# Performance work log

Measured on AMD Instinct MI355X. Metric: run time of the kernel, lower is better.

Reference implementation:

```python
import jax, jax.numpy as jnp
import numpy as np
from jax import lax

BN_INV = float(1.0 / np.sqrt(1.0 + 1e-5))  # BatchNorm eval: running_mean=0, running_var=1


def _block(x, w, b, g, beta, stride):
    # Conv3x3(stride, pad=1) -> BN(eval) -> ReLU -> MaxPool2
    x = lax.conv_general_dilated(x, w, (stride, stride), [(1, 1), (1, 1)],
                                 dimension_numbers=('NCHW', 'OIHW', 'NCHW'))
    x = x + b[None, :, None, None]
    x = x * (g * BN_INV)[None, :, None, None] + beta[None, :, None, None]
    x = jax.nn.relu(x)
    return lax.reduce_window(x, -jnp.inf, lax.max, (1, 1, 2, 2), (1, 1, 2, 2), 'VALID')


def _gru(x, wi, wh, bi, bh):
    # torch-style GRU, batch_first. x: (B, T, D)
    B = x.shape[0]
    H = wh.shape[1]

    def step(h, xt):
        gi = xt @ wi.T + bi
        gh = h @ wh.T + bh
        ir, iz, inn = jnp.split(gi, 3, axis=1)
        hr, hz, hn = jnp.split(gh, 3, axis=1)
        r = jax.nn.sigmoid(ir + hr)
        z = jax.nn.sigmoid(iz + hz)
        nn_ = jnp.tanh(inn + r * hn)
        h2 = (1.0 - z) * nn_ + z * h
        return h2, h2

    h0 = jnp.zeros((B, H), x.dtype)
    _, ys = lax.scan(step, h0, jnp.swapaxes(x, 0, 1))
    return jnp.swapaxes(ys, 0, 1)  # (B, T, H)


def setup_inputs() -> dict:
    key = jax.random.key(0)
    ks = jax.random.split(key, 32)
    rn = lambda i, shape, s: jax.random.normal(ks[i], shape, jnp.float32) * s
    inp = {
        'support': rn(0, (5, 5, 1, 224, 224), 1.0),
        'query': rn(1, (15, 1, 224, 224), 1.0),
        'conv_w1': rn(2, (32, 1, 3, 3), 0.3), 'conv_b1': rn(3, (32,), 0.1),
        'conv_w2': rn(4, (64, 32, 3, 3), 0.06), 'conv_b2': rn(5, (64,), 0.1),
        'conv_w3': rn(6, (128, 64, 3, 3), 0.04), 'conv_b3': rn(7, (128,), 0.1),
        'conv_w4': rn(8, (256, 128, 3, 3), 0.03), 'conv_b4': rn(9, (256,), 0.1),
        'bn_g1': 1.0 + rn(10, (32,), 0.05), 'bn_be1': rn(11, (32,), 0.05),
        'bn_g2': 1.0 + rn(12, (64,), 0.05), 'bn_be2': rn(13, (64,), 0.05),
        'bn_g3': 1.0 + rn(14, (128,), 0.05), 'bn_be3': rn(15, (128,), 0.05),
        'bn_g4': 1.0 + rn(16, (256,), 0.05), 'bn_be4': rn(17, (256,), 0.05),
        'att_w': rn(18, (64, 256), 0.06), 'att_b': rn(19, (64,), 0.05),
        'gru_wi0': rn(20, (384, 512), 0.04), 'gru_wh0': rn(21, (384, 128), 0.08),
        'gru_bi0': rn(22, (384,), 0.05), 'gru_bh0': rn(23, (384,), 0.05),
        'gru_wi1': rn(24, (384, 128), 0.08), 'gru_wh1': rn(25, (384, 128), 0.08),
        'gru_bi1': rn(26, (384,), 0.05), 'gru_bh1': rn(27, (384,), 0.05),
        'trans_w': rn(28, (1, 128), 0.08), 'trans_b': rn(29, (1,), 0.05),
    }
    return inp


def reference(support, query, conv_w1, conv_b1, conv_w2, conv_b2, conv_w3, conv_b3,
              conv_w4, conv_b4, bn_g1, bn_be1, bn_g2, bn_be2, bn_g3, bn_be3,
              bn_g4, bn_be4, att_w, att_b, gru_wi0, gru_wh0, gru_bi0, gru_bh0,
              gru_wi1, gru_wh1, gru_bi1, gru_bh1, trans_w, trans_b):
    n, k, c, w = support.shape[0], support.shape[1], support.shape[2], support.shape[3]
    qk = query.shape[0]

    def enc(x):
        x = _block(x, conv_w1, conv_b1, bn_g1, bn_be1, 2)
        x = _block(x, conv_w2, conv_b2, bn_g2, bn_be2, 1)
        x = _block(x, conv_w3, conv_b3, bn_g3, bn_be3, 1)
        x = _block(x, conv_w4, conv_b4, bn_g4, bn_be4, 1)
        B, F_, H_, W_ = x.shape
        return x.reshape(B, F_, H_ * W_).transpose(0, 2, 1)  # (B, seq, feat)

    hf = enc(support.reshape(n * k, c, w, w))  # (nk, S, f)
    qf = enc(query)                            # (qk, T, f)

    # ItemQueryAttention: score[q,s,t,u] = sum_h tanh(W(q_t) * W(h_u))
    Wq = qf @ att_w.T + att_b  # (qk, T, h)
    Wh = hf @ att_w.T + att_b  # (nk, S, h)
    scores = jnp.tanh(Wq[:, None, :, None, :] * Wh[None, :, None, :, :]).sum(-1)  # (qk,nk,T,S)
    att = jax.nn.softmax(scores, axis=3)
    attended = jnp.einsum('qsTS,sSf->qsTf', att, hf)  # (qk, nk, T, f)

    T_, f = qf.shape[1], qf.shape[2]
    qrep = jnp.broadcast_to(qf[:, None], (qk, n * k, T_, f))
    x = jnp.concatenate([attended, qrep], axis=-1).reshape(qk * n * k, T_, 2 * f)

    h = _gru(x, gru_wi0, gru_wh0, gru_bi0, gru_bh0)
    h = _gru(h, gru_wi1, gru_wh1, gru_bi1, gru_bh1)

    logits = (h[:, -1, :] @ trans_w.T + trans_b).reshape(qk, n, k).sum(axis=2)  # (qk, n)
    return jax.nn.log_softmax(logits, axis=1)
```

## Files before the change

kernel.cpp:

```cpp
#include <hip/hip_runtime.h>
#include <hip/hip_bf16.h>
#include <math.h>

typedef unsigned short u16;
typedef unsigned int u32;
typedef __attribute__((ext_vector_type(8))) short bf16x8v;
typedef __attribute__((ext_vector_type(4))) float f32x4;

constexpr int NS = 25, NQ = 15, NB = 40;
constexpr int B3 = 375;
constexpr int T49 = 49;
constexpr float BN_INV = 0.9999950000374997f;

constexpr size_t A1_OFF    = 0;
constexpr size_t X2_OFF    = 16056320;
constexpr size_t P2_OFF    = 48168960;
constexpr size_t X3_OFF    = 0;
constexpr size_t P3_OFF    = 56197120;
constexpr size_t X4_OFF    = 16056320;
constexpr size_t FEATT_OFF = 60211200;
constexpr size_t PROJ_OFF  = 24084480;
constexpr size_t ATT_OFF   = 24586240;
constexpr size_t GI_OFF    = 62218240;
constexpr size_t Y0_OFF    = 0;
constexpr size_t HFIN_OFF  = 90442240;
constexpr size_t WBH_OFF   = 91027456;
constexpr size_t WBL_OFF   = 92325888;
constexpr size_t W2_E = 0;
constexpr size_t W3_E = 18432;
constexpr size_t W4_E = 92160;
constexpr size_t AW_E = 387072;
constexpr size_t WI0_E = 403456;
constexpr size_t WI1_E = 600064;

static __device__ __forceinline__ u16 f2b(float f) {
  __hip_bfloat16 h = __float2bfloat16(f);
  return *reinterpret_cast<u16*>(&h);
}
static __device__ __forceinline__ float b2f(u16 u) {
  return __uint_as_float((u32)u << 16);
}
static __device__ __forceinline__ void split8(const float* v, u32* hp, u32* lp) {
  u16 h[8], l[8];
#pragma unroll
  for (int j = 0; j < 8; ++j) {
    const u16 hb = f2b(v[j]);
    h[j] = hb;
    l[j] = f2b(v[j] - b2f(hb));
  }
#pragma unroll
  for (int j = 0; j < 4; ++j) {
    hp[j] = (u32)h[2 * j] | ((u32)h[2 * j + 1] << 16);
    lp[j] = (u32)l[2 * j] | ((u32)l[2 * j + 1] << 16);
  }
}
constexpr float LOG2E = 1.4426950408889634f;
static __device__ __forceinline__ float fsigmoid(float x) {
  return __builtin_amdgcn_rcpf(1.f + __builtin_amdgcn_exp2f(-x * LOG2E));
}
static __device__ __forceinline__ float ftanh(float x) {
  return 1.f - 2.f * __builtin_amdgcn_rcpf(__builtin_amdgcn_exp2f(x * (2.f * LOG2E)) + 1.f);
}

__global__ void cvt_split(const float* __restrict__ x, u16* __restrict__ oh,
                          u16* __restrict__ ol, int n) {
  int i = blockIdx.x * 256 + threadIdx.x;
  if (i >= n) return;
  const float v = x[i];
  const u16 h = f2b(v);
  oh[i] = h;
  ol[i] = f2b(v - b2f(h));
}
__global__ void cvt_conv_w_split(const float* __restrict__ w, u16* __restrict__ oh,
                                 u16* __restrict__ ol, int OC, int IC) {
  const int n = OC * IC * 9;
  int i = blockIdx.x * 256 + threadIdx.x;
  if (i >= n) return;
  const int oc = i / (IC * 9), rem = i % (IC * 9);
  const int e = rem / IC, ic = rem % IC;
  const int ky = e / 3, kx = e % 3;
  const float v = w[((size_t)(oc * IC + ic) * 3 + ky) * 3 + kx];
  const u16 h = f2b(v);
  oh[i] = h;
  ol[i] = f2b(v - b2f(h));
}

__global__ __launch_bounds__(256) void conv1_pool(
    const float* __restrict__ support, const float* __restrict__ query,
    const float* __restrict__ w1, const float* __restrict__ cb1,
    const float* __restrict__ g1, const float* __restrict__ be1,
    float* __restrict__ out) {
  __shared__ float wl[288], scl[32], shl[32], cbl[32];
  const int tid = threadIdx.x;
  for (int l = tid; l < 288; l += 256) wl[l] = w1[l];
  if (tid < 32) { scl[tid] = g1[tid] * BN_INV; shl[tid] = be1[tid]; cbl[tid] = cb1[tid]; }
  __syncthreads();
  const int oc = tid & 31;
  const int p = blockIdx.x * 8 + (tid >> 5);
  const int ox = p % 56, oy = (p / 56) % 56, b = p / 3136;
  const float* in_b = (b < NS) ? (support + (size_t)b * 50176)
                               : (query + (size_t)(b - NS) * 50176);
  const int iy0 = 4 * oy - 1, ix0 = 4 * ox - 1;
  float pat[5][5];
#pragma unroll
  for (int dy = 0; dy < 5; ++dy) {
    const int iy = iy0 + dy;
#pragma unroll
    for (int dx = 0; dx < 5; ++dx) {
      const int ix = ix0 + dx;
      pat[dy][dx] = (iy >= 0 && iy < 224 && ix >= 0 && ix < 224)
                        ? in_b[(size_t)iy * 224 + ix] : 0.f;
    }
  }
  const float* wp = &wl[oc * 9];
  float mx = 0.f;
#pragma unroll
  for (int py = 0; py < 2; ++py)
#pragma unroll
    for (int px = 0; px < 2; ++px) {
      float acc = 0.f;
#pragma unroll
      for (int ky = 0; ky < 3; ++ky)
#pragma unroll
        for (int kx = 0; kx < 3; ++kx)
          acc += pat[2 * py + ky][2 * px + kx] * wp[ky * 3 + kx];
      float v = (acc + cbl[oc]) * scl[oc] + shl[oc];
      mx = fmaxf(mx, v);
    }
  out[(size_t)p * 32 + oc] = mx;
}

__global__ void maxpool2_f32(const float* __restrict__ X, float* __restrict__ Y,
                             int Bn, int H, int W, int C) {
  const int OH = H >> 1, OW = W >> 1;
  const int cpr = C >> 2;
  const int chunks = Bn * OH * OW * cpr;
  for (int i = blockIdx.x * blockDim.x + threadIdx.x; i < chunks;
       i += gridDim.x * blockDim.x) {
    const int c4 = i % cpr, m = i / cpr;
    const int ox = m % OW, oy = (m / OW) % OH, b = m / (OW * OH);
    const size_t base = (((size_t)b * H + 2 * oy) * W + 2 * ox) * C + (c4 << 2);
    const float4 r0 = *(const float4*)&X[base];
    const float4 r1 = *(const float4*)&X[base + C];
    const float4 r2 = *(const float4*)&X[base + (size_t)W * C];
    const float4 r3 = *(const float4*)&X[base + (size_t)W * C + C];
    float4 o;
    o.x = fmaxf(fmaxf(r0.x, r1.x), fmaxf(r2.x, r3.x));
    o.y = fmaxf(fmaxf(r0.y, r1.y), fmaxf(r2.y, r3.y));
    o.z = fmaxf(fmaxf(r0.z, r1.z), fmaxf(r2.z, r3.z));
    o.w = fmaxf(fmaxf(r0.w, r1.w), fmaxf(r2.w, r3.w));
    *(float4*)&Y[(size_t)m * C + (c4 << 2)] = o;
  }
}

template <int AMODE, int EPI>
__global__ __launch_bounds__(256) void sgemm(
    const float* __restrict__ A, const float* __restrict__ A2, int M, int K,
    const u16* __restrict__ Bh, const u16* __restrict__ Bl,
    const float* __restrict__ p0, const float* __restrict__ p1,
    const float* __restrict__ p2, float* __restrict__ Cout, int ldc,
    int H, int W, int IC, int icb) {
  __shared__ u16 Ash[64][72], Asl[64][72];
  __shared__ u16 Bsh[64][72], Bsl[64][72];
  const int tid = threadIdx.x;
  const int lane = tid & 63, wv = tid >> 6;
  const int wy = wv >> 1, wx = wv & 1;
  const int n0 = blockIdx.x * 64, m0 = blockIdx.y * 64;
  f32x4 acc[2][2] = {{{0, 0, 0, 0}, {0, 0, 0, 0}}, {{0, 0, 0, 0}, {0, 0, 0, 0}}};
  for (int k0 = 0; k0 < K; k0 += 64) {
#pragma unroll
    for (int s = 0; s < 2; ++s) {
      const int c = s * 256 + tid;
      const int row = c >> 3, kc = (c & 7) << 3;
      const int gm = m0 + row, gk = k0 + kc;
      float4 x0 = {0, 0, 0, 0}, x1 = {0, 0, 0, 0};
      if (AMODE == 0) {
        if (gm < M && gk < K) {
          const float* p = A + (size_t)gm * K + gk;
          x0 = *(const float4*)p; x1 = *(const float4*)(p + 4);
        }
      } else if (AMODE == 1) {
        if (gm < M) {
          const float* p;
          if (gk < 256) {
            p = A + (size_t)gm * 256 + gk;
          } else {
            const int b = gm / T49, t = gm % T49, q = b / NS;
            p = A2 + (((size_t)(NS + q) * T49 + t) << 8) + (gk - 256);
          }
          x0 = *(const float4*)p; x1 = *(const float4*)(p + 4);
        }
      } else {
        if (gm < M && gk < K) {
          const int ox = gm % W, t_ = gm / W;
          const int oy = t_ % H, b = t_ / H;
          const int e = gk >> icb, ic = gk & (IC - 1);
          const int ky = e / 3, kx = e - 3 * (e / 3);
          const int iy = oy + ky - 1, ix = ox + kx - 1;
          if (iy >= 0 && iy < H && ix >= 0 && ix < W) {
            const float* p = A + (((size_t)b * H + iy) * W + ix) * IC + ic;
            x0 = *(const float4*)p; x1 = *(const float4*)(p + 4);
          }
        }
      }
      float v[8] = {x0.x, x0.y, x0.z, x0.w, x1.x, x1.y, x1.z, x1.w};
      u32 hp[4], lp[4];
      split8(v, hp, lp);
      *(uint4*)&Ash[row][kc] = *(uint4*)hp;
      *(uint4*)&Asl[row][kc] = *(uint4*)lp;
    }
#pragma unroll
    for (int s = 0; s < 2; ++s) {
      const int c = s * 256 + tid;
      const int row = c >> 3, kc = (c & 7) << 3;
      const int gk = k0 + kc;
      uint4 vh = {0u, 0u, 0u, 0u}, vl = {0u, 0u, 0u, 0u};
      if (gk < K) {
        vh = *(const uint4*)&Bh[(size_t)(n0 + row) * K + gk];
        vl = *(const uint4*)&Bl[(size_t)(n0 + row) * K + gk];
      }
      *(uint4*)&Bsh[row][kc] = vh;
      *(uint4*)&Bsl[row][kc] = vl;
    }
    __syncthreads();
#pragma unroll
    for (int kk = 0; kk < 64; kk += 32) {
      const int ko = kk + ((lane >> 4) << 3);
      const int ra0 = wy * 32 + (lane & 15), ra1 = ra0 + 16;
      const int rb0 = wx * 32 + (lane & 15), rb1 = rb0 + 16;
      bf16x8v a0h = *(const bf16x8v*)&Ash[ra0][ko];
      bf16x8v a1h = *(const bf16x8v*)&Ash[ra1][ko];
      bf16x8v b0h = *(const bf16x8v*)&Bsh[rb0][ko];
      bf16x8v b1h = *(const bf16x8v*)&Bsh[rb1][ko];
      bf16x8v a0l = *(const bf16x8v*)&Asl[ra0][ko];
      bf16x8v a1l = *(const bf16x8v*)&Asl[ra1][ko];
      bf16x8v b0l = *(const bf16x8v*)&Bsl[rb0][ko];
      bf16x8v b1l = *(const bf16x8v*)&Bsl[rb1][ko];
      acc[0][0] = __builtin_amdgcn_mfma_f32_16x16x32_bf16(a0h, b0h, acc[0][0], 0, 0, 0);
      acc[0][1] = __builtin_amdgcn_mfma_f32_16x16x32_bf16(a0h, b1h, acc[0][1], 0, 0, 0);
      acc[1][0] = __builtin_amdgcn_mfma_f32_16x16x32_bf16(a1h, b0h, acc[1][0], 0, 0, 0);
      acc[1][1] = __builtin_amdgcn_mfma_f32_16x16x32_bf16(a1h, b1h, acc[1][1], 0, 0, 0);
      acc[0][0] = __builtin_amdgcn_mfma_f32_16x16x32_bf16(a0h, b0l, acc[0][0], 0, 0, 0);
      acc[0][1] = __builtin_amdgcn_mfma_f32_16x16x32_bf16(a0h, b1l, acc[0][1], 0, 0, 0);
      acc[1][0] = __builtin_amdgcn_mfma_f32_16x16x32_bf16(a1h, b0l, acc[1][0], 0, 0, 0);
      acc[1][1] = __builtin_amdgcn_mfma_f32_16x16x32_bf16(a1h, b1l, acc[1][1], 0, 0, 0);
      acc[0][0] = __builtin_amdgcn_mfma_f32_16x16x32_bf16(a0l, b0h, acc[0][0], 0, 0, 0);
      acc[0][1] = __builtin_amdgcn_mfma_f32_16x16x32_bf16(a0l, b1h, acc[0][1], 0, 0, 0);
      acc[1][0] = __builtin_amdgcn_mfma_f32_16x16x32_bf16(a1l, b0h, acc[1][0], 0, 0, 0);
      acc[1][1] = __builtin_amdgcn_mfma_f32_16x16x32_bf16(a1l, b1h, acc[1][1], 0, 0, 0);
    }
    __syncthreads();
  }
#pragma unroll
  for (int r = 0; r < 2; ++r) {
#pragma unroll
    for (int c = 0; c < 2; ++c) {
      const int gn = n0 + wx * 32 + c * 16 + (lane & 15);
      float sc0 = 0.f, sh0 = 0.f;
      if (EPI == 0) { sc0 = p1[gn] * BN_INV; sh0 = p2[gn]; }
#pragma unroll
      for (int i = 0; i < 4; ++i) {
        const int gm = m0 + wy * 32 + r * 16 + ((lane >> 4) << 2) + i;
        if (gm >= M) continue;
        const float a = acc[r][c][i];
        if (EPI == 0) {
          Cout[(size_t)gm * ldc + gn] = fmaxf((a + p0[gn]) * sc0 + sh0, 0.f);
        } else {
          Cout[(size_t)gm * ldc + gn] = a + p0[gn];
        }
      }
    }
  }
}

__global__ __launch_bounds__(256) void attention_f32(
    const float* __restrict__ proj, const float* __restrict__ featT,
    float* __restrict__ attended) {
  __shared__ float WqT[64][9];
  __shared__ float WhT[64][51];
  __shared__ float sc[7][64];
  const int bid = blockIdx.x;
  const int qs = bid / 7, tg = bid - 7 * qs;
  const int q = qs / NS, s = qs - NS * q;
  const int tid = threadIdx.x;
  const float* pq = proj + ((size_t)(NS + q) * T49 + tg * 7) * 64;
  const float* ph = proj + (size_t)s * T49 * 64;
  for (int l = tid; l < 7 * 64; l += 256) WqT[l & 63][l >> 6] = pq[l];
  for (int l = tid; l < T49 * 64; l += 256) WhT[l & 63][l >> 6] = ph[l];
  __syncthreads();
  constexpr float C2LOG2E = 2.8853900817779268f;
  for (int e = tid; e < 343; e += 256) {
    const int tl = e / 49, u = e - 49 * tl;
    float a0 = 0.f, a1 = 0.f, a2 = 0.f, a3 = 0.f;
#pragma unroll
    for (int h = 0; h < 64; h += 4) {
      const float p0 = WqT[h + 0][tl] * WhT[h + 0][u];
      const float p1 = WqT[h + 1][tl] * WhT[h + 1][u];
      const float p2 = WqT[h + 2][tl] * WhT[h + 2][u];
      const float p3 = WqT[h + 3][tl] * WhT[h + 3][u];
      a0 += 1.f - 2.f * __builtin_amdgcn_rcpf(__builtin_amdgcn_exp2f(p0 * C2LOG2E) + 1.f);
      a1 += 1.f - 2.f * __builtin_amdgcn_rcpf(__builtin_amdgcn_exp2f(p1 * C2LOG2E) + 1.f);
      a2 += 1.f - 2.f * __builtin_amdgcn_rcpf(__builtin_amdgcn_exp2f(p2 * C2LOG2E) + 1.f);
      a3 += 1.f - 2.f * __builtin_amdgcn_rcpf(__builtin_amdgcn_exp2f(p3 * C2LOG2E) + 1.f);
    }
    sc[tl][u] = (a0 + a1) + (a2 + a3);
  }
  __syncthreads();
  if (tid < 56) {
    const int t = tid >> 3, g = tid & 7;
    float m = -3.4e38f;
    for (int u = g; u < T49; u += 8) m = fmaxf(m, sc[t][u]);
    m = fmaxf(m, __shfl_xor(m, 4));
    m = fmaxf(m, __shfl_xor(m, 2));
    m = fmaxf(m, __shfl_xor(m, 1));
    float ssum = 0.f;
    for (int u = g; u < T49; u += 8) {
      const float e = __builtin_amdgcn_exp2f((sc[t][u] - m) * LOG2E);
      sc[t][u] = e; ssum += e;
    }
    ssum += __shfl_xor(ssum, 4);
    ssum += __shfl_xor(ssum, 2);
    ssum += __shfl_xor(ssum, 1);
    const float inv = 1.f / ssum;
    for (int u = g; u < T49; u += 8) sc[t][u] *= inv;
  }
  __syncthreads();
  const float* fs = featT + (size_t)s * T49 * 256;
  float* outp = attended + ((size_t)qs * T49 + tg * 7) * 256;
  float acc[7] = {0.f, 0.f, 0.f, 0.f, 0.f, 0.f, 0.f};
  for (int u = 0; u < T49; ++u) {
    const float v = fs[u * 256 + tid];
#pragma unroll
    for (int i = 0; i < 7; ++i) acc[i] += sc[i][u] * v;
  }
#pragma unroll
  for (int i = 0; i < 7; ++i) outp[(size_t)i * 256 + tid] = acc[i];
}

constexpr int SPB = 8;
__global__ __launch_bounds__(512) void gru_mfma(
    const float* __restrict__ gi,
    const float* __restrict__ wh,
    const float* __restrict__ bh,
    float* __restrict__ y,
    int store_all) {
  __shared__ u16 hah[16][136], hal[16][136];
  __shared__ float ghs[SPB][384];
  __shared__ float hfl[SPB][128];
  const int tid = threadIdx.x;
  const int lane = tid & 63, wv = tid >> 6;
  const int r0 = blockIdx.x * SPB;
  bf16x8v Bhr[3][4], Blr[3][4];
#pragma unroll
  for (int f = 0; f < 3; ++f) {
    const int n = (wv * 3 + f) * 16 + (lane & 15);
#pragma unroll
    for (int kk = 0; kk < 4; ++kk) {
      const int k = kk * 32 + ((lane >> 4) << 3);
      const float* p = wh + (size_t)n * 128 + k;
      float v[8];
      *(float4*)&v[0] = *(const float4*)p;
      *(float4*)&v[4] = *(const float4*)(p + 4);
      u32 hp[4], lp[4];
      split8(v, hp, lp);
      Bhr[f][kk] = *(bf16x8v*)hp;
      Blr[f][kk] = *(bf16x8v*)lp;
    }
  }
  const int row0 = tid >> 7, j0 = tid & 127;
  const int row1 = (512 + tid) >> 7, j1 = tid & 127;
  int sq0 = r0 + row0; if (sq0 >= B3) sq0 = B3 - 1;
  int sq1 = r0 + row1; if (sq1 >= B3) sq1 = B3 - 1;
  const float bhr0 = bh[j0], bhz0 = bh[128 + j0], bhn0 = bh[256 + j0];
  const float bhr1 = bh[j1], bhz1 = bh[128 + j1], bhn1 = bh[256 + j1];
  const float* gib0 = gi + (size_t)sq0 * T49 * 384;
  const float* gib1 = gi + (size_t)sq1 * T49 * 384;
  for (int i = tid; i < 16 * 136; i += 512) { hah[i / 136][i % 136] = 0; hal[i / 136][i % 136] = 0; }
  for (int i = tid; i < SPB * 128; i += 512) hfl[i >> 7][i & 127] = 0.f;
  __syncthreads();
  const int ar = lane & 15, ko = (lane >> 4) << 3;
  float xr0c = gib0[j0], xz0c = gib0[128 + j0], xn0c = gib0[256 + j0];
  float xr1c = gib1[j1], xz1c = gib1[128 + j1], xn1c = gib1[256 + j1];
  for (int t = 0; t < T49; ++t) {
    const int tn = (t + 1 < T49) ? t + 1 : t;
    const float* g0n = gib0 + (size_t)tn * 384;
    const float* g1n = gib1 + (size_t)tn * 384;
    const float xr0n = g0n[j0], xz0n = g0n[128 + j0], xn0n = g0n[256 + j0];
    const float xr1n = g1n[j1], xz1n = g1n[128 + j1], xn1n = g1n[256 + j1];
    bf16x8v Ah[4], Al[4];
#pragma unroll
    for (int kk = 0; kk < 4; ++kk) {
      Ah[kk] = *(const bf16x8v*)&hah[ar][kk * 32 + ko];
      Al[kk] = *(const bf16x8v*)&hal[ar][kk * 32 + ko];
    }
#pragma unroll
    for (int f = 0; f < 3; ++f) {
      f32x4 acc = {0, 0, 0, 0};
#pragma unroll
      for (int kk = 0; kk < 4; ++kk)
        acc = __builtin_amdgcn_mfma_f32_16x16x32_bf16(Ah[kk], Bhr[f][kk], acc, 0, 0, 0);
#pragma unroll
      for (int kk = 0; kk < 4; ++kk)
        acc = __builtin_amdgcn_mfma_f32_16x16x32_bf16(Ah[kk], Blr[f][kk], acc, 0, 0, 0);
#pragma unroll
      for (int kk = 0; kk < 4; ++kk)
        acc = __builtin_amdgcn_mfma_f32_16x16x32_bf16(Al[kk], Bhr[f][kk], acc, 0, 0, 0);
      const int nc = (wv * 3 + f) * 16 + (lane & 15);
      const int rb = (lane >> 4) << 2;
      if (rb < SPB) {
#pragma unroll
        for (int i = 0; i < 4; ++i) ghs[rb + i][nc] = acc[i];
      }
    }
    __syncthreads();
    {
      const float r_ = fsigmoid(xr0c + ghs[row0][j0] + bhr0);
      const float z_ = fsigmoid(xz0c + ghs[row0][128 + j0] + bhz0);
      const float n_ = ftanh(xn0c + r_ * (ghs[row0][256 + j0] + bhn0));
      const float hn = (1.f - z_) * n_ + z_ * hfl[row0][j0];
      hfl[row0][j0] = hn;
      const u16 hb = f2b(hn);
      hah[row0][j0] = hb;
      hal[row0][j0] = f2b(hn - b2f(hb));
      if (r0 + row0 < B3) {
        if (store_all) y[((size_t)(r0 + row0) * T49 + t) * 128 + j0] = hn;
        else if (t == T49 - 1) y[(size_t)(r0 + row0) * 128 + j0] = hn;
      }
    }
    {
      const float r_ = fsigmoid(xr1c + ghs[row1][j1] + bhr1);
      const float z_ = fsigmoid(xz1c + ghs[row1][128 + j1] + bhz1);
      const float n_ = ftanh(xn1c + r_ * (ghs[row1][256 + j1] + bhn1));
      const float hn = (1.f - z_) * n_ + z_ * hfl[row1][j1];
      hfl[row1][j1] = hn;
      const u16 hb = f2b(hn);
      hah[row1][j1] = hb;
      hal[row1][j1] = f2b(hn - b2f(hb));
      if (r0 + row1 < B3) {
        if (store_all) y[((size_t)(r0 + row1) * T49 + t) * 128 + j1] = hn;
        else if (t == T49 - 1) y[(size_t)(r0 + row1) * 128 + j1] = hn;
      }
    }
    __syncthreads();
    xr0c = xr0n; xz0c = xz0n; xn0c = xn0n;
    xr1c = xr1n; xz1c = xz1n; xn1c = xn1n;
  }
}

__global__ __launch_bounds__(512) void head_kernel(
    const float* __restrict__ hf, const float* __restrict__ tw,
    const float* __restrict__ tb, float* __restrict__ out) {
  __shared__ float lg[B3];
  const int tid = threadIdx.x;
  if (tid < B3) {
    const float* h = hf + (size_t)tid * 128;
    float acc = tb[0];
    for (int k = 0; k < 128; ++k) acc += h[k] * tw[k];
    lg[tid] = acc;
  }
  __syncthreads();
  if (tid < NQ) {
    float cls[5];
#pragma unroll
    for (int n = 0; n < 5; ++n) {
      float s = 0.f;
#pragma unroll
      for (int k = 0; k < 5; ++k) s += lg[tid * 25 + n * 5 + k];
      cls[n] = s;
    }
    float m = cls[0];
#pragma unroll
    for (int n = 1; n < 5; ++n) m = fmaxf(m, cls[n]);
    float se = 0.f;
#pragma unroll
    for (int n = 0; n < 5; ++n) se += expf(cls[n] - m);
    const float lse = m + logf(se);
#pragma unroll
    for (int n = 0; n < 5; ++n) out[tid * 5 + n] = cls[n] - lse;
  }
}

extern "C" void kernel_launch(void* const* d_in, const int* in_sizes, int n_in,
                              void* d_out, int out_size, void* d_ws,
                              size_t ws_size, hipStream_t stream) {
  (void)in_sizes; (void)n_in; (void)out_size; (void)ws_size;
  const float* support = (const float*)d_in[0];
  const float* query   = (const float*)d_in[1];
  const float* cw1 = (const float*)d_in[2];  const float* cb1 = (const float*)d_in[3];
  const float* cw2 = (const float*)d_in[4];  const float* cb2 = (const float*)d_in[5];
  const float* cw3 = (const float*)d_in[6];  const float* cb3 = (const float*)d_in[7];
  const float* cw4 = (const float*)d_in[8];  const float* cb4 = (const float*)d_in[9];
  const float* g1  = (const float*)d_in[10]; const float* be1 = (const float*)d_in[11];
  const float* g2  = (const float*)d_in[12]; const float* be2 = (const float*)d_in[13];
  const float* g3  = (const float*)d_in[14]; const float* be3 = (const float*)d_in[15];
  const float* g4  = (const float*)d_in[16]; const float* be4 = (const float*)d_in[17];
  const float* aw  = (const float*)d_in[18]; const float* ab  = (const float*)d_in[19];
  const float* wi0 = (const float*)d_in[20]; const float* wh0 = (const float*)d_in[21];
  const float* bi0 = (const float*)d_in[22]; const float* bh0 = (const float*)d_in[23];
  const float* wi1 = (const float*)d_in[24]; const float* wh1 = (const float*)d_in[25];
  const float* bi1 = (const float*)d_in[26]; const float* bh1 = (const float*)d_in[27];
  const float* tw  = (const float*)d_in[28]; const float* tb  = (const float*)d_in[29];

  char* ws = (char*)d_ws;
  float* out = (float*)d_out;
  float* A1    = (float*)(ws + A1_OFF);
  float* X2    = (float*)(ws + X2_OFF);
  float* P2    = (float*)(ws + P2_OFF);
  float* X3    = (float*)(ws + X3_OFF);
  float* P3    = (float*)(ws + P3_OFF);
  float* X4    = (float*)(ws + X4_OFF);
  float* FEATT = (float*)(ws + FEATT_OFF);
  float* PROJ  = (float*)(ws + PROJ_OFF);
  float* ATT   = (float*)(ws + ATT_OFF);
  float* GI    = (float*)(ws + GI_OFF);
  float* Y0    = (float*)(ws + Y0_OFF);
  float* HFIN  = (float*)(ws + HFIN_OFF);
  u16* WBH = (u16*)(ws + WBH_OFF);
  u16* WBL = (u16*)(ws + WBL_OFF);

  cvt_conv_w_split<<<(64 * 288 + 255) / 256, 256, 0, stream>>>(cw2, WBH + W2_E, WBL + W2_E, 64, 32);
  cvt_conv_w_split<<<(128 * 576 + 255) / 256, 256, 0, stream>>>(cw3, WBH + W3_E, WBL + W3_E, 128, 64);
  cvt_conv_w_split<<<(256 * 1152 + 255) / 256, 256, 0, stream>>>(cw4, WBH + W4_E, WBL + W4_E, 256, 128);
  cvt_split<<<(64 * 256 + 255) / 256, 256, 0, stream>>>(aw, WBH + AW_E, WBL + AW_E, 64 * 256);
  cvt_split<<<(384 * 512 + 255) / 256, 256, 0, stream>>>(wi0, WBH + WI0_E, WBL + WI0_E, 384 * 512);
  cvt_split<<<(384 * 128 + 255) / 256, 256, 0, stream>>>(wi1, WBH + WI1_E, WBL + WI1_E, 384 * 128);

  conv1_pool<<<15680, 256, 0, stream>>>(support, query, cw1, cb1, g1, be1, A1);
  sgemm<2, 0><<<dim3(1, 1960), 256, 0, stream>>>(
      A1, nullptr, 125440, 288, WBH + W2_E, WBL + W2_E, cb2, g2, be2, X2, 64,
      56, 56, 32, 5);
  maxpool2_f32<<<1960, 256, 0, stream>>>(X2, P2, NB, 56, 56, 64);
  sgemm<2, 0><<<dim3(2, 490), 256, 0, stream>>>(
      P2, nullptr, 31360, 576, WBH + W3_E, WBL + W3_E, cb3, g3, be3, X3, 128,
      28, 28, 64, 6);
  maxpool2_f32<<<980, 256, 0, stream>>>(X3, P3, NB, 28, 28, 128);
  sgemm<2, 0><<<dim3(4, 123), 256, 0, stream>>>(
      P3, nullptr, 7840, 1152, WBH + W4_E, WBL + W4_E, cb4, g4, be4, X4, 256,
      14, 14, 128, 7);
  maxpool2_f32<<<490, 256, 0, stream>>>(X4, FEATT, NB, 14, 14, 256);

  sgemm<0, 1><<<dim3(1, 31), 256, 0, stream>>>(
      FEATT, nullptr, NB * T49, 256, WBH + AW_E, WBL + AW_E, ab, nullptr,
      nullptr, PROJ, 64, 0, 0, 0, 0);
  attention_f32<<<B3 * 7, 256, 0, stream>>>(PROJ, FEATT, ATT);

  sgemm<1, 1><<<dim3(6, 288), 256, 0, stream>>>(
      ATT, FEATT, B3 * T49, 512, WBH + WI0_E, WBL + WI0_E, bi0, nullptr,
      nullptr, GI, 384, 0, 0, 0, 0);
  gru_mfma<<<47, 512, 0, stream>>>(GI, wh0, bh0, Y0, 1);
  sgemm<0, 1><<<dim3(6, 288), 256, 0, stream>>>(
      Y0, nullptr, B3 * T49, 128, WBH + WI1_E, WBL + WI1_E, bi1, nullptr,
      nullptr, GI, 384, 0, 0, 0, 0);
  gru_mfma<<<47, 512, 0, stream>>>(GI, wh1, bh1, HFIN, 0);

  head_kernel<<<1, 512, 0, stream>>>(HFIN, tw, tb, out);
}
```

Before: 405.0 us.

## Restructure GRU recurrence to compute gates in MFMA registers with double-buffered hidden state

The GRU kernel now assigns each wave 16 hidden units across all three gates, so the r/z/n accumulators for a lane land in registers and the gate math runs straight from MFMA outputs instead of going through a shared ghs buffer. The hidden state is double-buffered in shared memory, which cuts the per-timestep barriers from two to one, and the previous h is kept in registers. Each block now processes 16 sequences instead of 8, using all MFMA rows and halving the grid to 24 blocks. The trade-off is fewer blocks, so less of the GPU is used during this latency-bound serial recurrence.

```diff
diff --git a/kernel.cpp b/kernel.cpp
--- a/kernel.cpp
+++ b/kernel.cpp
@@ -337,113 +337,106 @@
   for (int i = 0; i < 7; ++i) outp[(size_t)i * 256 + tid] = acc[i];
 }
 
-constexpr int SPB = 8;
 __global__ __launch_bounds__(512) void gru_mfma(
     const float* __restrict__ gi,
     const float* __restrict__ wh,
     const float* __restrict__ bh,
     float* __restrict__ y,
     int store_all) {
-  __shared__ u16 hah[16][136], hal[16][136];
-  __shared__ float ghs[SPB][384];
-  __shared__ float hfl[SPB][128];
+  __shared__ u16 hah[2][16][136], hal[2][16][136];
   const int tid = threadIdx.x;
   const int lane = tid & 63, wv = tid >> 6;
-  const int r0 = blockIdx.x * SPB;
+  const int r0 = blockIdx.x * 16;
+  const int c = lane & 15, rq = lane >> 4;
+  const int j = wv * 16 + c;
+  const int ko = rq << 3;
   bf16x8v Bhr[3][4], Blr[3][4];
 #pragma unroll
-  for (int f = 0; f < 3; ++f) {
-    const int n = (wv * 3 + f) * 16 + (lane & 15);
+  for (int g = 0; g < 3; ++g) {
 #pragma unroll
     for (int kk = 0; kk < 4; ++kk) {
-      const int k = kk * 32 + ((lane >> 4) << 3);
-      const float* p = wh + (size_t)n * 128 + k;
+      const float* p = wh + (size_t)(g * 128 + j) * 128 + kk * 32 + ko;
       float v[8];
       *(float4*)&v[0] = *(const float4*)p;
       *(float4*)&v[4] = *(const float4*)(p + 4);
       u32 hp[4], lp[4];
       split8(v, hp, lp);
-      Bhr[f][kk] = *(bf16x8v*)hp;
-      Blr[f][kk] = *(bf16x8v*)lp;
-    }
-  }
-  const int row0 = tid >> 7, j0 = tid & 127;
-  const int row1 = (512 + tid) >> 7, j1 = tid & 127;
-  int sq0 = r0 + row0; if (sq0 >= B3) sq0 = B3 - 1;
-  int sq1 = r0 + row1; if (sq1 >= B3) sq1 = B3 - 1;
-  const float bhr0 = bh[j0], bhz0 = bh[128 + j0], bhn0 = bh[256 + j0];
-  const float bhr1 = bh[j1], bhz1 = bh[128 + j1], bhn1 = bh[256 + j1];
-  const float* gib0 = gi + (size_t)sq0 * T49 * 384;
-  const float* gib1 = gi + (size_t)sq1 * T49 * 384;
-  for (int i = tid; i < 16 * 136; i += 512) { hah[i / 136][i % 136] = 0; hal[i / 136][i % 136] = 0; }
-  for (int i = tid; i < SPB * 128; i += 512) hfl[i >> 7][i & 127] = 0.f;
+      Bhr[g][kk] = *(bf16x8v*)hp;
+      Blr[g][kk] = *(bf16x8v*)lp;
+    }
+  }
+  const float bh0 = bh[j], bh1 = bh[128 + j], bh2 = bh[256 + j];
+  int seqs[4];
+#pragma unroll
+  for (int i = 0; i < 4; ++i) {
+    const int s_ = r0 + rq * 4 + i;
+    seqs[i] = s_ < B3 ? s_ : B3 - 1;
+  }
+  for (int i = tid; i < 2 * 16 * 136; i += 512) {
+    ((u16*)hah)[i] = 0; ((u16*)hal)[i] = 0;
+  }
+  float hprev[4] = {0.f, 0.f, 0.f, 0.f};
   __syncthreads();
-  const int ar = lane & 15, ko = (lane >> 4) << 3;
-  float xr0c = gib0[j0], xz0c = gib0[128 + j0], xn0c = gib0[256 + j0];
-  float xr1c = gib1[j1], xz1c = gib1[128 + j1], xn1c = gib1[256 + j1];
+  float x0[4], x1[4], x2[4];
+#pragma unroll
+  for (int i = 0; i < 4; ++i) {
+    const float* g = gi + (size_t)seqs[i] * T49 * 384 + j;
+    x0[i] = g[0]; x1[i] = g[128]; x2[i] = g[256];
+  }
   for (int t = 0; t < T49; ++t) {
+    const int pr = t & 1, pw = pr ^ 1;
     const int tn = (t + 1 < T49) ? t + 1 : t;
-    const float* g0n = gib0 + (size_t)tn * 384;
-    const float* g1n = gib1 + (size_t)tn * 384;
-    const float xr0n = g0n[j0], xz0n = g0n[128 + j0], xn0n = g0n[256 + j0];
-    const float xr1n = g1n[j1], xz1n = g1n[128 + j1], xn1n = g1n[256 + j1];
+    float y0[4], y1[4], y2[4];
+#pragma unroll
+    for (int i = 0; i < 4; ++i) {
+      const float* g = gi + ((size_t)seqs[i] * T49 + tn) * 384 + j;
+      y0[i] = g[0]; y1[i] = g[128]; y2[i] = g[256];
+    }
     bf16x8v Ah[4], Al[4];
 #pragma unroll
     for (int kk = 0; kk < 4; ++kk) {
-      Ah[kk] = *(const bf16x8v*)&hah[ar][kk * 32 + ko];
-      Al[kk] = *(const bf16x8v*)&hal[ar][kk * 32 + ko];
-    }
-#pragma unroll
-    for (int f = 0; f < 3; ++f) {
-      f32x4 acc = {0, 0, 0, 0};
-#pragma unroll
-      for (int kk = 0; kk < 4; ++kk)
-        acc = __builtin_amdgcn_mfma_f32_16x16x32_bf16(Ah[kk], Bhr[f][kk], acc, 0, 0, 0);
-#pragma unroll
-      for (int kk = 0; kk < 4; ++kk)
-        acc = __builtin_amdgcn_mfma_f32_16x16x32_bf16(Ah[kk], Blr[f][kk], acc, 0, 0, 0);
-#pragma unroll
-      for (int kk = 0; kk < 4; ++kk)
-        acc = __builtin_amdgcn_mfma_f32_16x16x32_bf16(Al[kk], Bhr[f][kk], acc, 0, 0, 0);
-      const int nc = (wv * 3 + f) * 16 + (lane & 15);
-      const int rb = (lane >> 4) << 2;
-      if (rb < SPB) {
-#pragma unroll
-        for (int i = 0; i < 4; ++i) ghs[rb + i][nc] = acc[i];
+      Ah[kk] = *(const bf16x8v*)&hah[pr][c][kk * 32 + ko];
+      Al[kk] = *(const bf16x8v*)&hal[pr][c][kk * 32 + ko];
+    }
+    f32x4 aR = {0, 0, 0, 0}, aZ = {0, 0, 0, 0}, aN = {0, 0, 0, 0};
+#pragma unroll
+    for (int kk = 0; kk < 4; ++kk) {
+      aR = __builtin_amdgcn_mfma_f32_16x16x32_bf16(Ah[kk], Bhr[0][kk], aR, 0, 0, 0);
+      aZ = __builtin_amdgcn_mfma_f32_16x16x32_bf16(Ah[kk], Bhr[1][kk], aZ, 0, 0, 0);
+      aN = __builtin_amdgcn_mfma_f32_16x16x32_bf16(Ah[kk], Bhr[2][kk], aN, 0, 0, 0);
+    }
+#pragma unroll
+    for (int kk = 0; kk < 4; ++kk) {
+      aR = __builtin_amdgcn_mfma_f32_16x16x32_bf16(Ah[kk], Blr[0][kk], aR, 0, 0, 0);
+      aZ = __builtin_amdgcn_mfma_f32_16x16x32_bf16(Ah[kk], Blr[1][kk], aZ, 0, 0, 0);
+      aN = __builtin_amdgcn_mfma_f32_16x16x32_bf16(Ah[kk], Blr[2][kk], aN, 0, 0, 0);
+    }
+#pragma unroll
+    for (int kk = 0; kk < 4; ++kk) {
+      aR = __builtin_amdgcn_mfma_f32_16x16x32_bf16(Al[kk], Bhr[0][kk], aR, 0, 0, 0);
+      aZ = __builtin_amdgcn_mfma_f32_16x16x32_bf16(Al[kk], Bhr[1][kk], aZ, 0, 0, 0);
+      aN = __builtin_amdgcn_mfma_f32_16x16x32_bf16(Al[kk], Bhr[2][kk], aN, 0, 0, 0);
+    }
+#pragma unroll
+    for (int i = 0; i < 4; ++i) {
+      const int row = rq * 4 + i;
+      const float r_ = fsigmoid(x0[i] + aR[i] + bh0);
+      const float z_ = fsigmoid(x1[i] + aZ[i] + bh1);
+      const float n_ = ftanh(x2[i] + r_ * (aN[i] + bh2));
+      const float hn = (1.f - z_) * n_ + z_ * hprev[i];
+      hprev[i] = hn;
+      const u16 hb = f2b(hn);
+      hah[pw][row][j] = hb;
+      hal[pw][row][j] = f2b(hn - b2f(hb));
+      const int seq = r0 + row;
+      if (seq < B3) {
+        if (store_all) y[((size_t)seq * T49 + t) * 128 + j] = hn;
+        else if (t == T49 - 1) y[(size_t)seq * 128 + j] = hn;
       }
     }
     __syncthreads();
-    {
-      const float r_ = fsigmoid(xr0c + ghs[row0][j0] + bhr0);
-      const float z_ = fsigmoid(xz0c + ghs[row0][128 + j0] + bhz0);
-      const float n_ = ftanh(xn0c + r_ * (ghs[row0][256 + j0] + bhn0));
-      const float hn = (1.f - z_) * n_ + z_ * hfl[row0][j0];
-      hfl[row0][j0] = hn;
-      const u16 hb = f2b(hn);
-      hah[row0][j0] = hb;
-      hal[row0][j0] = f2b(hn - b2f(hb));
-      if (r0 + row0 < B3) {
-        if (store_all) y[((size_t)(r0 + row0) * T49 + t) * 128 + j0] = hn;
-        else if (t == T49 - 1) y[(size_t)(r0 + row0) * 128 + j0] = hn;
-      }
-    }
-    {
-      const float r_ = fsigmoid(xr1c + ghs[row1][j1] + bhr1);
-      const float z_ = fsigmoid(xz1c + ghs[row1][128 + j1] + bhz1);
-      const float n_ = ftanh(xn1c + r_ * (ghs[row1][256 + j1] + bhn1));
-      const float hn = (1.f - z_) * n_ + z_ * hfl[row1][j1];
-      hfl[row1][j1] = hn;
-      const u16 hb = f2b(hn);
-      hah[row1][j1] = hb;
-      hal[row1][j1] = f2b(hn - b2f(hb));
-      if (r0 + row1 < B3) {
-        if (store_all) y[((size_t)(r0 + row1) * T49 + t) * 128 + j1] = hn;
-        else if (t == T49 - 1) y[(size_t)(r0 + row1) * 128 + j1] = hn;
-      }
-    }
-    __syncthreads();
-    xr0c = xr0n; xz0c = xz0n; xn0c = xn0n;
-    xr1c = xr1n; xz1c = xz1n; xn1c = xn1n;
+#pragma unroll
+    for (int i = 0; i < 4; ++i) { x0[i] = y0[i]; x1[i] = y1[i]; x2[i] = y2[i]; }
   }
 }
 
@@ -547,11 +540,11 @@
   sgemm<1, 1><<<dim3(6, 288), 256, 0, stream>>>(
       ATT, FEATT, B3 * T49, 512, WBH + WI0_E, WBL + WI0_E, bi0, nullptr,
       nullptr, GI, 384, 0, 0, 0, 0);
-  gru_mfma<<<47, 512, 0, stream>>>(GI, wh0, bh0, Y0, 1);
+  gru_mfma<<<24, 512, 0, stream>>>(GI, wh0, bh0, Y0, 1);
   sgemm<0, 1><<<dim3(6, 288), 256, 0, stream>>>(
       Y0, nullptr, B3 * T49, 128, WBH + WI1_E, WBL + WI1_E, bi1, nullptr,
       nullptr, GI, 384, 0, 0, 0, 0);
-  gru_mfma<<<47, 512, 0, stream>>>(GI, wh1, bh1, HFIN, 0);
+  gru_mfma<<<24, 512, 0, stream>>>(GI, wh1, bh1, HFIN, 0);
 
   head_kernel<<<1, 512, 0, stream>>>(HFIN, tw, tb, out);
 }
```

Result: no change. 409.5 us (+1.1%).
